# Kernel tuning notes

Hardware: AMD Instinct MI355X
Metric: run time of the kernel (lower is better)

The kernel has to match this reference:

```python
import jax, jax.numpy as jnp
import numpy as np


def causal_fft_conv(v, h):
    # v: [B, L, D], h: [L, D]; causal (linear, not circular) conv via zero-padded FFT
    L = v.shape[1]
    n = 2 * L
    Vf = jnp.fft.rfft(v, n=n, axis=1)          # [B, n//2+1, D]
    Hf = jnp.fft.rfft(h, n=n, axis=0)          # [n//2+1, D]
    y = jnp.fft.irfft(Vf * Hf[None], n=n, axis=1)
    return y[:, :L].astype(v.dtype)


def setup_inputs() -> dict:
    key = jax.random.key(0)
    ks = jax.random.split(key, 5)
    B, L, D = 4, 4096, 1024
    scale = 1.0 / np.sqrt(D)
    x = jax.random.normal(ks[0], (B, L, D), dtype=jnp.float32)
    Wu = jax.random.normal(ks[1], (D, D), dtype=jnp.float32) * scale
    Wv = jax.random.normal(ks[2], (D, D), dtype=jnp.float32) * scale
    Wo = jax.random.normal(ks[3], (D, D), dtype=jnp.float32) * scale
    h_filter = jax.random.normal(ks[4], (L, D), dtype=jnp.float32) * 0.02
    bu = jnp.zeros((D,), jnp.float32)
    bv = jnp.zeros((D,), jnp.float32)
    bo = jnp.zeros((D,), jnp.float32)
    return {"x": x, "Wu": Wu, "bu": bu, "Wv": Wv, "bv": bv,
            "h_filter": h_filter, "Wo": Wo, "bo": bo}


def reference(x, Wu, bu, Wv, bv, h_filter, Wo, bo):
    L = x.shape[1]
    u = jnp.einsum('bld,de->ble', x, Wu) + bu
    v = jnp.einsum('bld,de->ble', x, Wv) + bv
    t = jnp.arange(L, dtype=x.dtype)
    decay = jnp.exp(-0.01 * t)[:, None]          # [L, 1]
    h = h_filter * decay                          # [L, D]
    v_conv = causal_fft_conv(v, h)                # [B, L, D]
    y = u * v_conv
    y = jnp.einsum('bld,de->ble', y, Wo) + bo
    return y
```

## Files before the change

kernel.cpp:

```cpp
#include <hip/hip_runtime.h>
#include <hip/hip_bf16.h>
#include <hip/hip_fp16.h>
#include <string.h>

typedef __hip_bfloat16 bf16;
typedef _Float16 f16;
typedef __attribute__((ext_vector_type(8))) short short8;
typedef __attribute__((ext_vector_type(4))) float floatx4;
typedef __attribute__((ext_vector_type(4))) unsigned int uintx4;

#define GLD16(gp, lp) __builtin_amdgcn_global_load_lds( \
    (__attribute__((address_space(1))) void*)(gp),      \
    (__attribute__((address_space(3))) void*)(lp), 16, 0, 0)

__device__ __forceinline__ unsigned short bf16_bits(float f) {
  bf16 h = (bf16)f;
  unsigned short s;
  memcpy(&s, &h, 2);
  return s;
}
__device__ __forceinline__ __half2 u2h2(unsigned u) {
  __half2 h;
  memcpy(&h, &u, 4);
  return h;
}

__global__ __launch_bounds__(256)
void cvtx_k(const float* __restrict__ x, char* __restrict__ outbase,
            size_t bstride) {
  size_t e = ((size_t)blockIdx.x * 256 + threadIdx.x) * 8;
  int b = (int)(e >> 22);
  size_t i = e & 4194303;
  const floatx4* s = (const floatx4*)(x + e);
  floatx4 a0 = s[0], a1 = s[1];
  union { uintx4 u4; unsigned short us[8]; } w;
  w.us[0] = bf16_bits(a0.x); w.us[1] = bf16_bits(a0.y);
  w.us[2] = bf16_bits(a0.z); w.us[3] = bf16_bits(a0.w);
  w.us[4] = bf16_bits(a1.x); w.us[5] = bf16_bits(a1.y);
  w.us[6] = bf16_bits(a1.z); w.us[7] = bf16_bits(a1.w);
  *(uintx4*)((bf16*)(outbase + (size_t)b * bstride) + i) = w.u4;
}

__global__ __launch_bounds__(256)
void transpose_k(const float* __restrict__ W0, const float* __restrict__ W1,
                 const float* __restrict__ W2, bf16* __restrict__ T0,
                 bf16* __restrict__ T1, bf16* __restrict__ T2) {
  __shared__ bf16 t[64][66];
  const float* S = blockIdx.z == 0 ? W0 : (blockIdx.z == 1 ? W1 : W2);
  bf16* Dst      = blockIdx.z == 0 ? T0 : (blockIdx.z == 1 ? T1 : T2);
  const int tx = threadIdx.x & 63, ty = threadIdx.x >> 6;
  const int kb = blockIdx.y * 64, nb = blockIdx.x * 64;
#pragma unroll
  for (int rr = 0; rr < 16; ++rr) {
    int r = ty * 16 + rr;
    t[r][tx] = (bf16)S[(size_t)(kb + r) * 1024 + nb + tx];
  }
  __syncthreads();
#pragma unroll
  for (int rr = 0; rr < 16; ++rr) {
    int r = ty * 16 + rr;
    Dst[(size_t)(nb + r) * 1024 + kb + tx] = t[tx][r];
  }
}

__global__ __launch_bounds__(256)
void hprep_k(const float* __restrict__ hf, f16* __restrict__ hp) {
  int idx = blockIdx.x * 256 + threadIdx.x;
  int dblk = idx >> 15;
  int rem = idx & 32767;
  int k = rem >> 6, dd = rem & 63;
  int d = dblk * 64 + dd;
  float val = hf[(size_t)k * 1024 + d] * __expf(-0.01f * (float)k);
  hp[idx] = (f16)val;
}

__device__ __forceinline__
void gemm_body(const bf16* __restrict__ A, const bf16* __restrict__ Bt,
               const float* __restrict__ bias, void* __restrict__ Cout,
               int out_mode, int m0, int n0) {
  constexpr int K = 1024;
  __shared__ __align__(16) bf16 As[128 * 32];
  __shared__ __align__(16) bf16 Bs[128 * 32];
  const int tid = threadIdx.x;
  const int lane = tid & 63;
  const int wave = tid >> 6;
  const int wm = wave >> 1, wn = wave & 1;
  const int r = lane & 15, q = lane >> 4;

  floatx4 acc[4][4] = {};

  const int s0 = tid, s1 = 256 + tid;
  const bf16* gA0 = A + (size_t)(m0 + (s0 >> 2)) * K + (s0 & 3) * 8;
  const bf16* gA1 = A + (size_t)(m0 + (s1 >> 2)) * K + (s1 & 3) * 8;
  const bf16* gB0 = Bt + (size_t)(n0 + (s0 >> 2)) * K + (s0 & 3) * 8;
  const bf16* gB1 = Bt + (size_t)(n0 + (s1 >> 2)) * K + (s1 & 3) * 8;
  char* AsB = (char*)As + wave * 1024;
  char* BsB = (char*)Bs + wave * 1024;

  for (int k0 = 0; k0 < K; k0 += 32) {
    GLD16(gA0 + k0, AsB);
    GLD16(gA1 + k0, AsB + 4096);
    GLD16(gB0 + k0, BsB);
    GLD16(gB1 + k0, BsB + 4096);
    __syncthreads();
    short8 af[4], bfr[4];
#pragma unroll
    for (int i = 0; i < 4; ++i)
      af[i] = *(const short8*)&As[(wm * 64 + i * 16 + r) * 32 + q * 8];
#pragma unroll
    for (int i = 0; i < 4; ++i)
      bfr[i] = *(const short8*)&Bs[(wn * 64 + i * 16 + r) * 32 + q * 8];
#pragma unroll
    for (int mi = 0; mi < 4; ++mi)
#pragma unroll
      for (int ni = 0; ni < 4; ++ni)
        acc[mi][ni] = __builtin_amdgcn_mfma_f32_16x16x32_bf16(
            af[mi], bfr[ni], acc[mi][ni], 0, 0, 0);
    __syncthreads();
  }

  const int cb = n0 + wn * 64;
  float bvv[4];
#pragma unroll
  for (int ni = 0; ni < 4; ++ni) bvv[ni] = bias[cb + ni * 16 + r];
#pragma unroll
  for (int mi = 0; mi < 4; ++mi) {
    int rowb = m0 + wm * 64 + mi * 16 + q * 4;
#pragma unroll
    for (int ni = 0; ni < 4; ++ni) {
      int col = cb + ni * 16 + r;
#pragma unroll
      for (int v = 0; v < 4; ++v) {
        float val = acc[mi][ni][v] + bvv[ni];
        size_t off = (size_t)(rowb + v) * 1024 + col;
        if (out_mode == 0)      ((bf16*)Cout)[off] = (bf16)val;
        else if (out_mode == 1) ((f16*)Cout)[off] = (f16)val;
        else                    ((float*)Cout)[off] = val;
      }
    }
  }
}

__global__ __launch_bounds__(256)
void gemm_uv_k(const bf16* __restrict__ A, const bf16* __restrict__ WuT,
               const bf16* __restrict__ WvT, const float* __restrict__ bu,
               const float* __restrict__ bv, bf16* __restrict__ u_out,
               f16* __restrict__ v_out) {
  const int isv = blockIdx.z;
  gemm_body(A, isv ? WvT : WuT, isv ? bv : bu,
            isv ? (void*)v_out : (void*)u_out, isv,
            blockIdx.x * 128, blockIdx.y * 128);
}

__global__ __launch_bounds__(256)
void gemm_o_k(const bf16* __restrict__ A, const bf16* __restrict__ Bt,
              const float* __restrict__ bias, float* __restrict__ C) {
  gemm_body(A, Bt, bias, (void*)C, 2, blockIdx.x * 128, blockIdx.y * 128);
}

__global__ __launch_bounds__(256)
void conv_k(const f16* __restrict__ vg0, const f16* __restrict__ hp,
            bf16* __restrict__ up0) {
  constexpr int CC = 64, TT = 128, D = 1024;
  __shared__ __align__(16) unsigned vs2[(TT + CC) * 32];
  __shared__ __align__(16) unsigned hs2[CC * 32];
  const int tid = threadIdx.x;
  const int pp = tid & 31, tg = tid >> 5;
  const int bx = blockIdx.x;
  const int t0 = blockIdx.y * TT;
  const int base = tg * 16;
  const unsigned* vg32 = (const unsigned*)(vg0 + (size_t)blockIdx.z * 4096 * D);
  unsigned* up32 = (unsigned*)(up0 + (size_t)blockIdx.z * 4096 * D);
  const uintx4* vg4 = (const uintx4*)vg32;
  const uintx4* hp4 = (const uintx4*)hp + (size_t)bx * 512 * 8;

  float ax[16], ay[16];
#pragma unroll
  for (int i = 0; i < 16; ++i) { ax[i] = 0.f; ay[i] = 0.f; }

  for (int c = 0; c < 8; ++c) {
    const int k0 = c * CC;
    __syncthreads();
    {
      uintx4* hd = (uintx4*)hs2;
      hd[tid] = hp4[k0 * 8 + tid];
      hd[tid + 256] = hp4[k0 * 8 + tid + 256];
    }
    {
      uintx4* vd = (uintx4*)vs2;
#pragma unroll
      for (int it = 0; it < 6; ++it) {
        int q = it * 256 + tid;
        int row = q >> 3, dp4 = q & 7;
        int tau = t0 - k0 - CC + row;
        uintx4 val = {0, 0, 0, 0};
        if (tau >= 0) val = vg4[(size_t)tau * 128 + bx * 8 + dp4];
        vd[q] = val;
      }
    }
    __syncthreads();

    __half2 p[16];
#pragma unroll
    for (int i = 0; i < 16; ++i)
      p[i] = u2h2(vs2[(base + i + CC) * 32 + pp]);
    __half2 acc2[16];
    const __half2 z2 = __float2half2_rn(0.f);
#pragma unroll
    for (int i = 0; i < 16; ++i) acc2[i] = z2;

    for (int kb = 0; kb < 4; ++kb) {
#pragma unroll
      for (int k2 = 0; k2 < 16; ++k2) {
        const int kk = kb * 16 + k2;
        __half2 hk = u2h2(hs2[kk * 32 + pp]);
#pragma unroll
        for (int i = 0; i < 16; ++i)
          acc2[i] = __hfma2(hk, p[(i - k2) & 15], acc2[i]);
        p[(15 - k2) & 15] = u2h2(vs2[(base + CC - 1 - kk) * 32 + pp]);
      }
    }
#pragma unroll
    for (int i = 0; i < 16; ++i) {
      ax[i] += __low2float(acc2[i]);
      ay[i] += __high2float(acc2[i]);
    }
  }

  const size_t rb = (size_t)(t0 + base) * 512 + bx * 32 + pp;
#pragma unroll
  for (int i = 0; i < 16; ++i) {
    unsigned uw = up32[rb + (size_t)i * 512];
    float ul = __uint_as_float((uw & 0xffffu) << 16);
    float uh = __uint_as_float(uw & 0xffff0000u);
    unsigned lo = bf16_bits(ul * ax[i]);
    unsigned hi = bf16_bits(uh * ay[i]);
    up32[rb + (size_t)i * 512] = lo | (hi << 16);
  }
}

extern "C" void kernel_launch(void* const* d_in, const int* in_sizes, int n_in,
                              void* d_out, int out_size, void* d_ws,
                              size_t ws_size, hipStream_t stream) {
  const float* x  = (const float*)d_in[0];
  const float* Wu = (const float*)d_in[1];
  const float* bu = (const float*)d_in[2];
  const float* Wv = (const float*)d_in[3];
  const float* bv = (const float*)d_in[4];
  const float* hf = (const float*)d_in[5];
  const float* Wo = (const float*)d_in[6];
  const float* bo = (const float*)d_in[7];
  char* ws = (char*)d_ws;
  bf16* WuT = (bf16*)(ws);
  bf16* WvT = (bf16*)(ws + 2097152);
  bf16* WoT = (bf16*)(ws + 4194304);
  f16*  hp  = (f16*)(ws + 6291456);

  dim3 tb(256);
  transpose_k<<<dim3(16, 16, 3), tb, 0, stream>>>(Wu, Wv, Wo, WuT, WvT, WoT);
  hprep_k<<<dim3(2048), tb, 0, stream>>>(hf, hp);

  if (ws_size >= 42991616ull) {
    bf16* xb = (bf16*)d_out;
    f16*  vf = (f16*)((char*)d_out + 33554432);
    bf16* u  = (bf16*)(ws + 8388608);
    cvtx_k<<<dim3(8192), tb, 0, stream>>>(x, (char*)d_out, 8388608);
    gemm_uv_k<<<dim3(128, 8, 2), tb, 0, stream>>>(xb, WuT, WvT, bu, bv, u, vf);
    conv_k<<<dim3(16, 32, 4), tb, 0, stream>>>(vf, hp, u);
    gemm_o_k<<<dim3(128, 8), tb, 0, stream>>>(u, WoT, bo, (float*)d_out);
  } else {
    bf16* u_b = (bf16*)(ws + 8388608);
    cvtx_k<<<dim3(8192), tb, 0, stream>>>(x, (char*)d_out, 16777216);
    for (int b = 0; b < 4; ++b) {
      char* quarter = (char*)d_out + (size_t)b * 16777216;
      bf16* xb = (bf16*)quarter;
      f16*  vb = (f16*)(quarter + 8388608);
      float* outb = (float*)d_out + (size_t)b * 4194304;
      gemm_uv_k<<<dim3(32, 8, 2), tb, 0, stream>>>(xb, WuT, WvT, bu, bv,
                                                   u_b, vb);
      conv_k<<<dim3(16, 32, 1), tb, 0, stream>>>(vb, hp, u_b);
      gemm_o_k<<<dim3(32, 8), tb, 0, stream>>>(u_b, WoT, bo, outb);
    }
  }
}
```

Baseline: 433.6 us.

## Prefetch next conv chunk into registers and carry sliding window across chunks

The conv kernel now loads the next chunk's v and h tiles from global memory into registers while the current chunk is being computed, then stores them to shared memory at the top of the following iteration. This overlaps global-load latency with the FMA loop. The sliding-window register array p is loaded from shared memory only on the first chunk and carried across chunks, because after 64 shifts it already holds the rows the next chunk needs. A min-blocks hint of 4 is added to launch bounds. The 32 extra staging registers per thread plus that occupancy target may force the compiler to spill.

Result: no change. 434.4 us (+0.2%).

```diff
diff --git a/kernel.cpp b/kernel.cpp
--- a/kernel.cpp
+++ b/kernel.cpp
@@ -158,7 +158,7 @@
   gemm_body(A, Bt, bias, (void*)C, 2, blockIdx.x * 128, blockIdx.y * 128);
 }
 
-__global__ __launch_bounds__(256)
+__global__ __launch_bounds__(256, 4)
 void conv_k(const f16* __restrict__ vg0, const f16* __restrict__ hp,
             bf16* __restrict__ up0) {
   constexpr int CC = 64, TT = 128, D = 1024;
@@ -178,32 +178,53 @@
 #pragma unroll
   for (int i = 0; i < 16; ++i) { ax[i] = 0.f; ay[i] = 0.f; }
 
+  uintx4 vstg[6], hstg[2];
+#pragma unroll
+  for (int it = 0; it < 6; ++it) {
+    int q = it * 256 + tid;
+    int row = q >> 3, dp4 = q & 7;
+    int tau = t0 - CC + row;
+    uintx4 val = {0, 0, 0, 0};
+    if (tau >= 0) val = vg4[(size_t)tau * 128 + bx * 8 + dp4];
+    vstg[it] = val;
+  }
+  hstg[0] = hp4[tid];
+  hstg[1] = hp4[tid + 256];
+
+  __half2 p[16];
+
   for (int c = 0; c < 8; ++c) {
-    const int k0 = c * CC;
     __syncthreads();
     {
+      uintx4* vd = (uintx4*)vs2;
+#pragma unroll
+      for (int it = 0; it < 6; ++it) vd[it * 256 + tid] = vstg[it];
       uintx4* hd = (uintx4*)hs2;
-      hd[tid] = hp4[k0 * 8 + tid];
-      hd[tid + 256] = hp4[k0 * 8 + tid + 256];
-    }
-    {
-      uintx4* vd = (uintx4*)vs2;
+      hd[tid] = hstg[0];
+      hd[tid + 256] = hstg[1];
+    }
+    __syncthreads();
+    if (c < 7) {
+      const int k0n = (c + 1) * CC;
 #pragma unroll
       for (int it = 0; it < 6; ++it) {
         int q = it * 256 + tid;
         int row = q >> 3, dp4 = q & 7;
-        int tau = t0 - k0 - CC + row;
+        int tau = t0 - k0n - CC + row;
         uintx4 val = {0, 0, 0, 0};
         if (tau >= 0) val = vg4[(size_t)tau * 128 + bx * 8 + dp4];
-        vd[q] = val;
+        vstg[it] = val;
       }
-    }
-    __syncthreads();
-
-    __half2 p[16];
-#pragma unroll
-    for (int i = 0; i < 16; ++i)
-      p[i] = u2h2(vs2[(base + i + CC) * 32 + pp]);
+      hstg[0] = hp4[k0n * 8 + tid];
+      hstg[1] = hp4[k0n * 8 + tid + 256];
+    }
+
+    if (c == 0) {
+#pragma unroll
+      for (int i = 0; i < 16; ++i)
+        p[i] = u2h2(vs2[(base + i + CC) * 32 + pp]);
+    }
+
     __half2 acc2[16];
     const __half2 z2 = __float2half2_rn(0.f);
 #pragma unroll
```

## Use 256x256 GEMM tiles with double-buffered LDS, XOR swizzle and 512 threads

Applied to the files above, without the earlier changes.

Replaces the 128x128, single-buffered, BK=32 GEMM body with a 256x256 tile, BK=64 and 512 threads (8 waves, each computing 128x64). The next K-tile is prefetched into a second LDS buffer while the current one is consumed, and an XOR swizzle on the LDS layout is meant to cut bank conflicts. The goals are better operand reuse, fewer barriers and hidden global-load latency for the three projection GEMMs. In exchange, LDS use rises to 128KB per block and each thread holds 128 accumulator floats, so occupancy is lower, and the grid shrinks to 256-512 blocks, which may underfill the CUs.

After: 421.4 us. 2.8% less time.

```diff
diff --git a/kernel.cpp b/kernel.cpp
--- a/kernel.cpp
+++ b/kernel.cpp
@@ -75,63 +75,113 @@
 }
 
 __device__ __forceinline__
-void gemm_body(const bf16* __restrict__ A, const bf16* __restrict__ Bt,
-               const float* __restrict__ bias, void* __restrict__ Cout,
-               int out_mode, int m0, int n0) {
+void gemm_body256(const bf16* __restrict__ A, const bf16* __restrict__ Bt,
+                  const float* __restrict__ bias, void* __restrict__ Cout,
+                  int out_mode, int m0, int n0) {
   constexpr int K = 1024;
-  __shared__ __align__(16) bf16 As[128 * 32];
-  __shared__ __align__(16) bf16 Bs[128 * 32];
+  __shared__ __align__(16) bf16 Asl[2][16384];
+  __shared__ __align__(16) bf16 Bsl[2][16384];
   const int tid = threadIdx.x;
   const int lane = tid & 63;
   const int wave = tid >> 6;
-  const int wm = wave >> 1, wn = wave & 1;
-  const int r = lane & 15, q = lane >> 4;
-
-  floatx4 acc[4][4] = {};
-
-  const int s0 = tid, s1 = 256 + tid;
-  const bf16* gA0 = A + (size_t)(m0 + (s0 >> 2)) * K + (s0 & 3) * 8;
-  const bf16* gA1 = A + (size_t)(m0 + (s1 >> 2)) * K + (s1 & 3) * 8;
-  const bf16* gB0 = Bt + (size_t)(n0 + (s0 >> 2)) * K + (s0 & 3) * 8;
-  const bf16* gB1 = Bt + (size_t)(n0 + (s1 >> 2)) * K + (s1 & 3) * 8;
-  char* AsB = (char*)As + wave * 1024;
-  char* BsB = (char*)Bs + wave * 1024;
-
-  for (int k0 = 0; k0 < K; k0 += 32) {
-    GLD16(gA0 + k0, AsB);
-    GLD16(gA1 + k0, AsB + 4096);
-    GLD16(gB0 + k0, BsB);
-    GLD16(gB1 + k0, BsB + 4096);
-    __syncthreads();
-    short8 af[4], bfr[4];
-#pragma unroll
-    for (int i = 0; i < 4; ++i)
-      af[i] = *(const short8*)&As[(wm * 64 + i * 16 + r) * 32 + q * 8];
-#pragma unroll
-    for (int i = 0; i < 4; ++i)
-      bfr[i] = *(const short8*)&Bs[(wn * 64 + i * 16 + r) * 32 + q * 8];
-#pragma unroll
-    for (int mi = 0; mi < 4; ++mi)
-#pragma unroll
-      for (int ni = 0; ni < 4; ++ni)
-        acc[mi][ni] = __builtin_amdgcn_mfma_f32_16x16x32_bf16(
-            af[mi], bfr[ni], acc[mi][ni], 0, 0, 0);
+  const int wm = wave >> 2, wn = wave & 3;
+  const int r = lane & 15, qlane = lane >> 4;
+
+  floatx4 acc[8][4] = {};
+
+  const bf16* gA[4];
+  const bf16* gB[4];
+#pragma unroll
+  for (int is = 0; is < 4; ++is) {
+    int p = is * 512 + tid;
+    int m = p >> 3;
+    int qe = (p & 7) ^ (m & 7);
+    gA[is] = A  + (size_t)(m0 + m) * K + qe * 8;
+    gB[is] = Bt + (size_t)(n0 + m) * K + qe * 8;
+  }
+  const int wbyte = wave * 1024;
+
+  const int rx = r & 7;
+  const int aRow = (wm * 128 + r) * 128;
+  const int bRow = (wn * 64 + r) * 128;
+  const int a0off = aRow + ((qlane) ^ rx) * 16;
+  const int a1off = aRow + ((4 + qlane) ^ rx) * 16;
+  const int b0off = bRow + ((qlane) ^ rx) * 16;
+  const int b1off = bRow + ((4 + qlane) ^ rx) * 16;
+
+#pragma unroll
+  for (int is = 0; is < 4; ++is)
+    GLD16(gA[is], (char*)&Asl[0][0] + is * 8192 + wbyte);
+#pragma unroll
+  for (int is = 0; is < 4; ++is)
+    GLD16(gB[is], (char*)&Bsl[0][0] + is * 8192 + wbyte);
+  __syncthreads();
+
+  for (int kt = 0; kt < 16; ++kt) {
+    const int cur = kt & 1;
+    const char* Ab = (const char*)&Asl[cur][0];
+    const char* Bb = (const char*)&Bsl[cur][0];
+
+    if (kt < 15) {
+      const int k0 = (kt + 1) * 64;
+#pragma unroll
+      for (int is = 0; is < 4; ++is)
+        GLD16(gA[is] + k0, (char*)&Asl[cur ^ 1][0] + is * 8192 + wbyte);
+#pragma unroll
+      for (int is = 0; is < 4; ++is)
+        GLD16(gB[is] + k0, (char*)&Bsl[cur ^ 1][0] + is * 8192 + wbyte);
+    }
+
+    {
+      short8 af[8], bfr[4];
+#pragma unroll
+      for (int i = 0; i < 8; ++i)
+        af[i] = *(const short8*)(Ab + a0off + i * 2048);
+#pragma unroll
+      for (int j = 0; j < 4; ++j)
+        bfr[j] = *(const short8*)(Bb + b0off + j * 2048);
+      __builtin_amdgcn_s_setprio(1);
+#pragma unroll
+      for (int i = 0; i < 8; ++i)
+#pragma unroll
+        for (int j = 0; j < 4; ++j)
+          acc[i][j] = __builtin_amdgcn_mfma_f32_16x16x32_bf16(
+              af[i], bfr[j], acc[i][j], 0, 0, 0);
+      __builtin_amdgcn_s_setprio(0);
+    }
+    {
+      short8 af[8], bfr[4];
+#pragma unroll
+      for (int i = 0; i < 8; ++i)
+        af[i] = *(const short8*)(Ab + a1off + i * 2048);
+#pragma unroll
+      for (int j = 0; j < 4; ++j)
+        bfr[j] = *(const short8*)(Bb + b1off + j * 2048);
+      __builtin_amdgcn_s_setprio(1);
+#pragma unroll
+      for (int i = 0; i < 8; ++i)
+#pragma unroll
+        for (int j = 0; j < 4; ++j)
+          acc[i][j] = __builtin_amdgcn_mfma_f32_16x16x32_bf16(
+              af[i], bfr[j], acc[i][j], 0, 0, 0);
+      __builtin_amdgcn_s_setprio(0);
+    }
     __syncthreads();
   }
 
   const int cb = n0 + wn * 64;
   float bvv[4];
 #pragma unroll
-  for (int ni = 0; ni < 4; ++ni) bvv[ni] = bias[cb + ni * 16 + r];
-#pragma unroll
-  for (int mi = 0; mi < 4; ++mi) {
-    int rowb = m0 + wm * 64 + mi * 16 + q * 4;
-#pragma unroll
-    for (int ni = 0; ni < 4; ++ni) {
-      int col = cb + ni * 16 + r;
+  for (int j = 0; j < 4; ++j) bvv[j] = bias[cb + j * 16 + r];
+#pragma unroll
+  for (int i = 0; i < 8; ++i) {
+    int rowb = m0 + wm * 128 + i * 16 + qlane * 4;
+#pragma unroll
+    for (int j = 0; j < 4; ++j) {
+      int col = cb + j * 16 + r;
 #pragma unroll
       for (int v = 0; v < 4; ++v) {
-        float val = acc[mi][ni][v] + bvv[ni];
+        float val = acc[i][j][v] + bvv[j];
         size_t off = (size_t)(rowb + v) * 1024 + col;
         if (out_mode == 0)      ((bf16*)Cout)[off] = (bf16)val;
         else if (out_mode == 1) ((f16*)Cout)[off] = (f16)val;
@@ -141,21 +191,21 @@
   }
 }
 
-__global__ __launch_bounds__(256)
+__global__ __launch_bounds__(512, 2)
 void gemm_uv_k(const bf16* __restrict__ A, const bf16* __restrict__ WuT,
                const bf16* __restrict__ WvT, const float* __restrict__ bu,
                const float* __restrict__ bv, bf16* __restrict__ u_out,
                f16* __restrict__ v_out) {
   const int isv = blockIdx.z;
-  gemm_body(A, isv ? WvT : WuT, isv ? bv : bu,
-            isv ? (void*)v_out : (void*)u_out, isv,
-            blockIdx.x * 128, blockIdx.y * 128);
-}
-
-__global__ __launch_bounds__(256)
+  gemm_body256(A, isv ? WvT : WuT, isv ? bv : bu,
+               isv ? (void*)v_out : (void*)u_out, isv,
+               blockIdx.x * 256, blockIdx.y * 256);
+}
+
+__global__ __launch_bounds__(512, 2)
 void gemm_o_k(const bf16* __restrict__ A, const bf16* __restrict__ Bt,
               const float* __restrict__ bias, float* __restrict__ C) {
-  gemm_body(A, Bt, bias, (void*)C, 2, blockIdx.x * 128, blockIdx.y * 128);
+  gemm_body256(A, Bt, bias, (void*)C, 2, blockIdx.x * 256, blockIdx.y * 256);
 }
 
 __global__ __launch_bounds__(256)
@@ -257,6 +307,7 @@
   f16*  hp  = (f16*)(ws + 6291456);
 
   dim3 tb(256);
+  dim3 tg(512);
   transpose_k<<<dim3(16, 16, 3), tb, 0, stream>>>(Wu, Wv, Wo, WuT, WvT, WoT);
   hprep_k<<<dim3(2048), tb, 0, stream>>>(hf, hp);
 
@@ -265,9 +316,9 @@
     f16*  vf = (f16*)((char*)d_out + 33554432);
     bf16* u  = (bf16*)(ws + 8388608);
     cvtx_k<<<dim3(8192), tb, 0, stream>>>(x, (char*)d_out, 8388608);
-    gemm_uv_k<<<dim3(128, 8, 2), tb, 0, stream>>>(xb, WuT, WvT, bu, bv, u, vf);
+    gemm_uv_k<<<dim3(64, 4, 2), tg, 0, stream>>>(xb, WuT, WvT, bu, bv, u, vf);
     conv_k<<<dim3(16, 32, 4), tb, 0, stream>>>(vf, hp, u);
-    gemm_o_k<<<dim3(128, 8), tb, 0, stream>>>(u, WoT, bo, (float*)d_out);
+    gemm_o_k<<<dim3(64, 4), tg, 0, stream>>>(u, WoT, bo, (float*)d_out);
   } else {
     bf16* u_b = (bf16*)(ws + 8388608);
     cvtx_k<<<dim3(8192), tb, 0, stream>>>(x, (char*)d_out, 16777216);
@@ -276,10 +327,10 @@
       bf16* xb = (bf16*)quarter;
       f16*  vb = (f16*)(quarter + 8388608);
       float* outb = (float*)d_out + (size_t)b * 4194304;
-      gemm_uv_k<<<dim3(32, 8, 2), tb, 0, stream>>>(xb, WuT, WvT, bu, bv,
+      gemm_uv_k<<<dim3(16, 4, 2), tg, 0, stream>>>(xb, WuT, WvT, bu, bv,
                                                    u_b, vb);
       conv_k<<<dim3(16, 32, 1), tb, 0, stream>>>(vb, hp, u_b);
-      gemm_o_k<<<dim3(32, 8), tb, 0, stream>>>(u_b, WoT, bo, outb);
-    }
-  }
-}
+      gemm_o_k<<<dim3(16, 4), tg, 0, stream>>>(u_b, WoT, bo, outb);
+    }
+  }
+}
```

## Double-buffer GEMM LDS tiles with swizzle and 256x128 tiles on 512 threads

Applied to the files above, without the earlier changes.

Rewrites the shared GEMM body used by the u/v projection and output projection. Global-to-LDS loads are now double-buffered, so the next K slice is fetched while MFMAs run on the current one. The XOR swizzle on chunk positions is meant to avoid LDS bank conflicts, and s_setprio is raised around the MFMA burst. The block tile grows to 256x128 with 512 threads, giving fewer blocks and more reuse of each B tile. The cost is more LDS per block and fewer blocks in flight, and correctness depends on manual vmcnt waits.

Result: faster. 417.9 us (-3.6%).

```diff
diff --git a/kernel.cpp b/kernel.cpp
--- a/kernel.cpp
+++ b/kernel.cpp
@@ -75,63 +75,93 @@
 }
 
 __device__ __forceinline__
-void gemm_body(const bf16* __restrict__ A, const bf16* __restrict__ Bt,
-               const float* __restrict__ bias, void* __restrict__ Cout,
-               int out_mode, int m0, int n0) {
+void gemm_body_occ(const bf16* __restrict__ A, const bf16* __restrict__ Bt,
+                   const float* __restrict__ bias, void* __restrict__ Cout,
+                   int out_mode, int m0, int n0) {
   constexpr int K = 1024;
-  __shared__ __align__(16) bf16 As[128 * 32];
-  __shared__ __align__(16) bf16 Bs[128 * 32];
+  __shared__ __align__(16) bf16 Asl[2][8192];
+  __shared__ __align__(16) bf16 Bsl[2][4096];
   const int tid = threadIdx.x;
   const int lane = tid & 63;
   const int wave = tid >> 6;
   const int wm = wave >> 1, wn = wave & 1;
-  const int r = lane & 15, q = lane >> 4;
+  const int r = lane & 15, qlane = lane >> 4;
 
   floatx4 acc[4][4] = {};
 
-  const int s0 = tid, s1 = 256 + tid;
-  const bf16* gA0 = A + (size_t)(m0 + (s0 >> 2)) * K + (s0 & 3) * 8;
-  const bf16* gA1 = A + (size_t)(m0 + (s1 >> 2)) * K + (s1 & 3) * 8;
-  const bf16* gB0 = Bt + (size_t)(n0 + (s0 >> 2)) * K + (s0 & 3) * 8;
-  const bf16* gB1 = Bt + (size_t)(n0 + (s1 >> 2)) * K + (s1 & 3) * 8;
-  char* AsB = (char*)As + wave * 1024;
-  char* BsB = (char*)Bs + wave * 1024;
-
-  for (int k0 = 0; k0 < K; k0 += 32) {
-    GLD16(gA0 + k0, AsB);
-    GLD16(gA1 + k0, AsB + 4096);
-    GLD16(gB0 + k0, BsB);
-    GLD16(gB1 + k0, BsB + 4096);
-    __syncthreads();
+  const bf16* gA[2];
+#pragma unroll
+  for (int is = 0; is < 2; ++is) {
+    int p = is * 512 + tid;
+    int m = p >> 2;
+    int qe = (p & 3) ^ (m & 3);
+    gA[is] = A + (size_t)(m0 + m) * K + qe * 8;
+  }
+  const bf16* gB0;
+  {
+    int m = tid >> 2;
+    int qe = (tid & 3) ^ (m & 3);
+    gB0 = Bt + (size_t)(n0 + m) * K + qe * 8;
+  }
+  const int wbyte = wave * 1024;
+
+  const int rx3 = r & 3;
+  const int aRow = (wm * 64 + r) * 64;
+  const int bRow = (wn * 64 + r) * 64;
+  const int aoff = aRow + (qlane ^ rx3) * 16;
+  const int boff = bRow + (qlane ^ rx3) * 16;
+
+  GLD16(gA[0], (char*)&Asl[0][0] + wbyte);
+  GLD16(gA[1], (char*)&Asl[0][0] + 8192 + wbyte);
+  GLD16(gB0,  (char*)&Bsl[0][0] + wbyte);
+
+  for (int kt = 0; kt < 32; ++kt) {
+    const int cur = kt & 1;
+    const char* Ab = (const char*)&Asl[cur][0];
+    const char* Bb = (const char*)&Bsl[cur][0];
+
+    if (kt < 31) {
+      const int k0 = (kt + 1) * 32;
+      GLD16(gA[0] + k0, (char*)&Asl[cur ^ 1][0] + wbyte);
+      GLD16(gA[1] + k0, (char*)&Asl[cur ^ 1][0] + 8192 + wbyte);
+      GLD16(gB0  + k0, (char*)&Bsl[cur ^ 1][0] + wbyte);
+      asm volatile("s_waitcnt vmcnt(3)" ::: "memory");
+    } else {
+      asm volatile("s_waitcnt vmcnt(0)" ::: "memory");
+    }
+    __builtin_amdgcn_s_barrier();
+
     short8 af[4], bfr[4];
 #pragma unroll
     for (int i = 0; i < 4; ++i)
-      af[i] = *(const short8*)&As[(wm * 64 + i * 16 + r) * 32 + q * 8];
+      af[i] = *(const short8*)(Ab + aoff + i * 1024);
+#pragma unroll
+    for (int j = 0; j < 4; ++j)
+      bfr[j] = *(const short8*)(Bb + boff + j * 1024);
+    __builtin_amdgcn_s_setprio(1);
 #pragma unroll
     for (int i = 0; i < 4; ++i)
-      bfr[i] = *(const short8*)&Bs[(wn * 64 + i * 16 + r) * 32 + q * 8];
-#pragma unroll
-    for (int mi = 0; mi < 4; ++mi)
-#pragma unroll
-      for (int ni = 0; ni < 4; ++ni)
-        acc[mi][ni] = __builtin_amdgcn_mfma_f32_16x16x32_bf16(
-            af[mi], bfr[ni], acc[mi][ni], 0, 0, 0);
-    __syncthreads();
+#pragma unroll
+      for (int j = 0; j < 4; ++j)
+        acc[i][j] = __builtin_amdgcn_mfma_f32_16x16x32_bf16(
+            af[i], bfr[j], acc[i][j], 0, 0, 0);
+    __builtin_amdgcn_s_setprio(0);
+    __builtin_amdgcn_s_barrier();
   }
 
   const int cb = n0 + wn * 64;
   float bvv[4];
 #pragma unroll
-  for (int ni = 0; ni < 4; ++ni) bvv[ni] = bias[cb + ni * 16 + r];
-#pragma unroll
-  for (int mi = 0; mi < 4; ++mi) {
-    int rowb = m0 + wm * 64 + mi * 16 + q * 4;
-#pragma unroll
-    for (int ni = 0; ni < 4; ++ni) {
-      int col = cb + ni * 16 + r;
+  for (int j = 0; j < 4; ++j) bvv[j] = bias[cb + j * 16 + r];
+#pragma unroll
+  for (int i = 0; i < 4; ++i) {
+    int rowb = m0 + wm * 64 + i * 16 + qlane * 4;
+#pragma unroll
+    for (int j = 0; j < 4; ++j) {
+      int col = cb + j * 16 + r;
 #pragma unroll
       for (int v = 0; v < 4; ++v) {
-        float val = acc[mi][ni][v] + bvv[ni];
+        float val = acc[i][j][v] + bvv[j];
         size_t off = (size_t)(rowb + v) * 1024 + col;
         if (out_mode == 0)      ((bf16*)Cout)[off] = (bf16)val;
         else if (out_mode == 1) ((f16*)Cout)[off] = (f16)val;
@@ -141,21 +171,21 @@
   }
 }
 
-__global__ __launch_bounds__(256)
+__global__ __launch_bounds__(512, 4)
 void gemm_uv_k(const bf16* __restrict__ A, const bf16* __restrict__ WuT,
                const bf16* __restrict__ WvT, const float* __restrict__ bu,
                const float* __restrict__ bv, bf16* __restrict__ u_out,
                f16* __restrict__ v_out) {
   const int isv = blockIdx.z;
-  gemm_body(A, isv ? WvT : WuT, isv ? bv : bu,
-            isv ? (void*)v_out : (void*)u_out, isv,
-            blockIdx.x * 128, blockIdx.y * 128);
-}
-
-__global__ __launch_bounds__(256)
+  gemm_body_occ(A, isv ? WvT : WuT, isv ? bv : bu,
+                isv ? (void*)v_out : (void*)u_out, isv,
+                blockIdx.x * 256, blockIdx.y * 128);
+}
+
+__global__ __launch_bounds__(512, 4)
 void gemm_o_k(const bf16* __restrict__ A, const bf16* __restrict__ Bt,
               const float* __restrict__ bias, float* __restrict__ C) {
-  gemm_body(A, Bt, bias, (void*)C, 2, blockIdx.x * 128, blockIdx.y * 128);
+  gemm_body_occ(A, Bt, bias, (void*)C, 2, blockIdx.x * 256, blockIdx.y * 128);
 }
 
 __global__ __launch_bounds__(256)
@@ -257,6 +287,7 @@
   f16*  hp  = (f16*)(ws + 6291456);
 
   dim3 tb(256);
+  dim3 tg(512);
   transpose_k<<<dim3(16, 16, 3), tb, 0, stream>>>(Wu, Wv, Wo, WuT, WvT, WoT);
   hprep_k<<<dim3(2048), tb, 0, stream>>>(hf, hp);
 
@@ -265,9 +296,9 @@
     f16*  vf = (f16*)((char*)d_out + 33554432);
     bf16* u  = (bf16*)(ws + 8388608);
     cvtx_k<<<dim3(8192), tb, 0, stream>>>(x, (char*)d_out, 8388608);
-    gemm_uv_k<<<dim3(128, 8, 2), tb, 0, stream>>>(xb, WuT, WvT, bu, bv, u, vf);
+    gemm_uv_k<<<dim3(64, 8, 2), tg, 0, stream>>>(xb, WuT, WvT, bu, bv, u, vf);
     conv_k<<<dim3(16, 32, 4), tb, 0, stream>>>(vf, hp, u);
-    gemm_o_k<<<dim3(128, 8), tb, 0, stream>>>(u, WoT, bo, (float*)d_out);
+    gemm_o_k<<<dim3(64, 8), tg, 0, stream>>>(u, WoT, bo, (float*)d_out);
   } else {
     bf16* u_b = (bf16*)(ws + 8388608);
     cvtx_k<<<dim3(8192), tb, 0, stream>>>(x, (char*)d_out, 16777216);
@@ -276,10 +307,10 @@
       bf16* xb = (bf16*)quarter;
       f16*  vb = (f16*)(quarter + 8388608);
       float* outb = (float*)d_out + (size_t)b * 4194304;
-      gemm_uv_k<<<dim3(32, 8, 2), tb, 0, stream>>>(xb, WuT, WvT, bu, bv,
+      gemm_uv_k<<<dim3(16, 8, 2), tg, 0, stream>>>(xb, WuT, WvT, bu, bv,
                                                    u_b, vb);
       conv_k<<<dim3(16, 32, 1), tb, 0, stream>>>(vb, hp, u_b);
-      gemm_o_k<<<dim3(32, 8), tb, 0, stream>>>(u_b, WoT, bo, outb);
-    }
-  }
-}
+      gemm_o_k<<<dim3(16, 8), tg, 0, stream>>>(u_b, WoT, bo, outb);
+    }
+  }
+}
```
